# Kernel optimization log

Measured on AMD Instinct MI355X. Metric: run time of the kernel, lower is better.

Reference implementation:

```python
import jax, jax.numpy as jnp
import numpy as np

B, S, D = 2, 2048, 768
C = 8                # num_channels
R = D // C           # ternary_rank = 96 (RoPE head_dim)
THETA = 10000.0
TERNARY_STD = 0.2
TERNARY_SCALE = 1.0  # ternary_factor_scaling


def _rope_tables():
    # HF-style RoPE: inv_freq over half dim, emb = concat(freqs, freqs)
    inv_freq = 1.0 / (THETA ** (np.arange(0, R, 2, dtype=np.float32) / R))
    pos = np.arange(S, dtype=np.float32)
    freqs = pos[:, None] * inv_freq[None, :]          # [S, R/2]
    emb = np.concatenate([freqs, freqs], axis=-1)     # [S, R]
    cos = np.broadcast_to(np.cos(emb)[None], (B, S, R)).copy()
    sin = np.broadcast_to(np.sin(emb)[None], (B, S, R)).copy()
    return jnp.asarray(cos), jnp.asarray(sin)


def setup_inputs() -> dict:
    key = jax.random.key(0)
    k1, k2, k3 = jax.random.split(key, 3)
    qz = jax.random.normal(k1, (B, S, D), dtype=jnp.float32)
    U = jax.random.normal(k2, (D, D), dtype=jnp.float32) * TERNARY_STD
    V = jax.random.normal(k3, (D, D), dtype=jnp.float32) * TERNARY_STD
    cos, sin = _rope_tables()
    return {"qz": qz, "cos": cos, "sin": sin, "U": U, "V": V}


def _rotate_half(x):
    h = x.shape[-1] // 2
    return jnp.concatenate([-x[..., h:], x[..., :h]], axis=-1)


def reference(qz, cos, sin, U, V):
    # cos/sin: [B,S,R] -> broadcast over channel dim -> [B,1,S,R]
    cosb = cos[:, None, :, :]
    sinb = sin[:, None, :, :]
    rope = lambda x: x * cosb + _rotate_half(x) * sinb       # apply
    rope_o = lambda x: x * cosb - _rotate_half(x) * sinb     # apply_o (inverse)

    # projections: F.linear(qz, W) == qz @ W.T
    qz_u = (qz @ U.T * TERNARY_SCALE).reshape(B, S, C, R).transpose(0, 2, 1, 3)
    qz_v = (qz @ V.T * TERNARY_SCALE).reshape(B, S, C, R).transpose(0, 2, 1, 3)

    qz_uo = rope_o(qz_u)
    qz_ur = rope(qz_u)
    qz_vr = rope(qz_v)

    # message_F: [B,C,S,S]
    message_F = jnp.einsum('bcqr,bckr->bcqk', qz_ur, qz_vr)
    # softmax(message_F / regularize_h) with regularize_h = 1/D  ->  * D
    qh = jax.nn.softmax((message_F * jnp.float32(D)).astype(jnp.float32), axis=-1).astype(qz_ur.dtype)

    qh_v1 = rope_o(jnp.einsum('bcqk,bckr->bcqr', qh, qz_vr))  # qh @ qz_v
    qh_v2 = rope(jnp.einsum('bckq,bckr->bcqr', qh, qz_uo))    # qh^T @ qz_uo

    qh_v1 = qh_v1.transpose(0, 2, 1, 3).reshape(B, S, D)
    qh_v2 = qh_v2.transpose(0, 2, 1, 3).reshape(B, S, D)

    message_G = (qh_v1 @ U + qh_v2 @ V) * TERNARY_SCALE
    return message_G
```

## Files before the change

kernel.cpp:

```cpp
#include <hip/hip_runtime.h>

typedef _Float16 f16;
typedef _Float16 f16x8 __attribute__((ext_vector_type(8)));
typedef _Float16 f16x4 __attribute__((ext_vector_type(4)));
typedef float f32x4 __attribute__((ext_vector_type(4)));

#define MFMA16(A,B,C) __builtin_amdgcn_mfma_f32_16x16x32_f16(A,B,C,0,0,0)
#define INV2048 4.8828125e-4f
#define HN (16ll*2048*96)
#define UVN 589824
#define ZC1 1107.98979f
#define ZC2 0.54101064f

__device__ __forceinline__ void split_f16(float x, f16& h, f16& l) {
    h = (f16)x;
    l = (f16)((x - (float)h) * 2048.0f);
}

__global__ __launch_bounds__(256) void k0_split(const float* __restrict__ qz,
                                                const float* __restrict__ U,
                                                const float* __restrict__ V,
                                                f16* __restrict__ qzh, f16* __restrict__ qzl,
                                                f16* __restrict__ Uh, f16* __restrict__ Ul,
                                                f16* __restrict__ Vh, f16* __restrict__ Vl) {
    const int i4 = blockIdx.x * 256 + threadIdx.x;
    {
        float4 x = *(const float4*)(qz + (size_t)i4 * 4);
        f16 h0, l0, h1, l1, h2, l2, h3, l3;
        split_f16(x.x, h0, l0); split_f16(x.y, h1, l1);
        split_f16(x.z, h2, l2); split_f16(x.w, h3, l3);
        f16x4 hv = {h0, h1, h2, h3};
        f16x4 lv = {l0, l1, l2, l3};
        *(f16x4*)(qzh + (size_t)i4 * 4) = hv;
        *(f16x4*)(qzl + (size_t)i4 * 4) = lv;
    }
    if (i4 < UVN / 4) {
        float4 x = *(const float4*)(U + (size_t)i4 * 4);
        f16 h0, l0, h1, l1, h2, l2, h3, l3;
        split_f16(x.x, h0, l0); split_f16(x.y, h1, l1);
        split_f16(x.z, h2, l2); split_f16(x.w, h3, l3);
        f16x4 hv = {h0, h1, h2, h3};
        f16x4 lv = {l0, l1, l2, l3};
        *(f16x4*)(Uh + (size_t)i4 * 4) = hv;
        *(f16x4*)(Ul + (size_t)i4 * 4) = lv;
        float4 y = *(const float4*)(V + (size_t)i4 * 4);
        split_f16(y.x, h0, l0); split_f16(y.y, h1, l1);
        split_f16(y.z, h2, l2); split_f16(y.w, h3, l3);
        f16x4 hv2 = {h0, h1, h2, h3};
        f16x4 lv2 = {l0, l1, l2, l3};
        *(f16x4*)(Vh + (size_t)i4 * 4) = hv2;
        *(f16x4*)(Vl + (size_t)i4 * 4) = lv2;
    }
}

__global__ __launch_bounds__(256, 2) void k1_proj(const f16* __restrict__ qzh,
                                                  const f16* __restrict__ qzl,
                                                  const f16* __restrict__ Uh,
                                                  const f16* __restrict__ Ul,
                                                  const f16* __restrict__ Vh,
                                                  const f16* __restrict__ Vl,
                                                  const float* __restrict__ cosb,
                                                  const float* __restrict__ sinb,
                                                  f16* __restrict__ uhp, f16* __restrict__ ulp,
                                                  f16* __restrict__ vhp, f16* __restrict__ vlp,
                                                  f16* __restrict__ vT, f16* __restrict__ oT) {
    __shared__ __align__(16) f16 smem[36864];
    f16* sAh  = smem;
    f16* sAl  = smem + 4608;
    f16* sBuh = smem + 9216;
    f16* sBul = smem + 9216 + 6912;
    f16* sBvh = smem + 9216 + 2 * 6912;
    f16* sBvl = smem + 9216 + 3 * 6912;

    const int tid = threadIdx.x;
    const int w = tid >> 6, lane = tid & 63;
    const int quad = lane >> 4, l15 = lane & 15;
    const int wr = w >> 1, wc = w & 1;
    const int bs0 = blockIdx.x * 64;
    const int c = blockIdx.y;

    const f16* Ug_h = Uh + (size_t)c * 96 * 768;
    const f16* Ug_l = Ul + (size_t)c * 96 * 768;
    const f16* Vg_h = Vh + (size_t)c * 96 * 768;
    const f16* Vg_l = Vl + (size_t)c * 96 * 768;

    f32x4 aUS[2][3] = {}, aUX[2][3] = {};
    f32x4 aVS[2][3] = {}, aVX[2][3] = {};

    for (int k0 = 0; k0 < 768; k0 += 64) {
        __syncthreads();
#pragma unroll
        for (int m = 0; m < 2; ++m) {
            int f = tid + 256 * m, row = f >> 3, cg = f & 7;
            const size_t go = (size_t)(bs0 + row) * 768 + k0 + cg * 8;
            const int lo = row * 72 + cg * 8;
            *(float4*)&sAh[lo] = *(const float4*)(qzh + go);
            *(float4*)&sAl[lo] = *(const float4*)(qzl + go);
        }
#pragma unroll
        for (int m = 0; m < 3; ++m) {
            int f = tid + 256 * m, row = f >> 3, cg = f & 7;
            const size_t go = (size_t)row * 768 + k0 + cg * 8;
            const int lo = row * 72 + cg * 8;
            *(float4*)&sBuh[lo] = *(const float4*)(Ug_h + go);
            *(float4*)&sBul[lo] = *(const float4*)(Ug_l + go);
            *(float4*)&sBvh[lo] = *(const float4*)(Vg_h + go);
            *(float4*)&sBvl[lo] = *(const float4*)(Vg_l + go);
        }
        __syncthreads();
#pragma unroll
        for (int cc = 0; cc < 2; ++cc) {
            f16x8 ah[2], al[2];
#pragma unroll
            for (int mt = 0; mt < 2; ++mt) {
                const int ar = (32 * wr + 16 * mt + l15) * 72 + cc * 32 + quad * 8;
                ah[mt] = *(const f16x8*)&sAh[ar];
                al[mt] = *(const f16x8*)&sAl[ar];
            }
#pragma unroll
            for (int nt = 0; nt < 3; ++nt) {
                const int br = (48 * wc + 16 * nt + l15) * 72 + cc * 32 + quad * 8;
                f16x8 buh = *(const f16x8*)&sBuh[br];
                f16x8 bul = *(const f16x8*)&sBul[br];
                f16x8 bvh = *(const f16x8*)&sBvh[br];
                f16x8 bvl = *(const f16x8*)&sBvl[br];
#pragma unroll
                for (int mt = 0; mt < 2; ++mt) {
                    aUS[mt][nt] = MFMA16(ah[mt], buh, aUS[mt][nt]);
                    aUX[mt][nt] = MFMA16(ah[mt], bul, aUX[mt][nt]);
                    aUX[mt][nt] = MFMA16(al[mt], buh, aUX[mt][nt]);
                    aVS[mt][nt] = MFMA16(ah[mt], bvh, aVS[mt][nt]);
                    aVX[mt][nt] = MFMA16(ah[mt], bvl, aVX[mt][nt]);
                    aVX[mt][nt] = MFMA16(al[mt], bvh, aVX[mt][nt]);
                }
            }
        }
    }

    __syncthreads();
    float* LU = (float*)smem;
    float* LV = LU + 6400;
#pragma unroll
    for (int mt = 0; mt < 2; ++mt)
#pragma unroll
        for (int nt = 0; nt < 3; ++nt)
#pragma unroll
            for (int r = 0; r < 4; ++r) {
                const int sl = 32 * wr + 16 * mt + 4 * quad + r;
                const int col = 48 * wc + 16 * nt + l15;
                LU[sl * 100 + col] = aUS[mt][nt][r] + aUX[mt][nt][r] * INV2048;
                LV[sl * 100 + col] = aVS[mt][nt][r] + aVX[mt][nt][r] * INV2048;
            }
    __syncthreads();

    const int b = bs0 >> 11;
    const int s0 = bs0 & 2047;
    const int head = b * 8 + c;
    const size_t nb = (size_t)head * 2048 * 96;
    const size_t tb = (size_t)head * 96 * 2048;
    const int ty = tid >> 4, tx = tid & 15;

#pragma unroll
    for (int jj = 0; jj < 3; ++jj) {
        int r = tx + 16 * jj;
        f16 vt1[4], vt2[4], ot1[4], ot2[4];
#pragma unroll
        for (int ii = 0; ii < 4; ++ii) {
            int sl = 4 * ty + ii;
            int s = s0 + sl;
            int cbi = (b * 2048 + s) * 96 + r;
            float cc = cosb[cbi], ss = sinb[cbi];
            size_t rowb = nb + (size_t)s * 96;
            float u1 = LU[sl * 100 + r], u2 = LU[sl * 100 + r + 48];
            float v1 = LV[sl * 100 + r], v2 = LV[sl * 100 + r + 48];
            float ur1 = u1 * cc - u2 * ss, ur2 = u2 * cc + u1 * ss;
            float uo1 = u1 * cc + u2 * ss, uo2 = u2 * cc - u1 * ss;
            float vr1 = v1 * cc - v2 * ss, vr2 = v2 * cc + v1 * ss;
            f16 h, l;
            split_f16(ur1, h, l); uhp[rowb + r] = h;      ulp[rowb + r] = l;
            split_f16(ur2, h, l); uhp[rowb + r + 48] = h; ulp[rowb + r + 48] = l;
            split_f16(vr1, h, l); vhp[rowb + r] = h;      vlp[rowb + r] = l;      vt1[ii] = h;
            split_f16(vr2, h, l); vhp[rowb + r + 48] = h; vlp[rowb + r + 48] = l; vt2[ii] = h;
            ot1[ii] = (f16)uo1; ot2[ii] = (f16)uo2;
        }
        f16x4 pv1 = {vt1[0], vt1[1], vt1[2], vt1[3]};
        f16x4 pv2 = {vt2[0], vt2[1], vt2[2], vt2[3]};
        f16x4 po1 = {ot1[0], ot1[1], ot1[2], ot1[3]};
        f16x4 po2 = {ot2[0], ot2[1], ot2[2], ot2[3]};
        *(f16x4*)&vT[tb + (size_t)r * 2048 + s0 + 4 * ty] = pv1;
        *(f16x4*)&vT[tb + (size_t)(r + 48) * 2048 + s0 + 4 * ty] = pv2;
        *(f16x4*)&oT[tb + (size_t)r * 2048 + s0 + 4 * ty] = po1;
        *(f16x4*)&oT[tb + (size_t)(r + 48) * 2048 + s0 + 4 * ty] = po2;
    }
}

__global__ __launch_bounds__(256, 2) void k2_stats(const f16* __restrict__ uhp,
                                                   const f16* __restrict__ ulp,
                                                   const f16* __restrict__ vhp,
                                                   const f16* __restrict__ vlp,
                                                   float* __restrict__ Mo,
                                                   float* __restrict__ Lo) {
    __shared__ f16 Bh[64 * 104];
    __shared__ f16 Bl[64 * 104];
    __shared__ float Mbuf[4][64], Lbuf[4][64];
    const int tid = threadIdx.x, w = tid >> 6, lane = tid & 63;
    const int quad = lane >> 4, l15 = lane & 15;
    const int q0 = blockIdx.x * 64, head = blockIdx.y;
    const f16* Ah_g = uhp + (size_t)head * 2048 * 96;
    const f16* Al_g = ulp + (size_t)head * 2048 * 96;
    const f16* Bh_g = vhp + (size_t)head * 2048 * 96;
    const f16* Bl_g = vlp + (size_t)head * 2048 * 96;

    f16x8 Afh[4][3], Afl[4][3];
#pragma unroll
    for (int mt = 0; mt < 4; ++mt)
#pragma unroll
        for (int cc = 0; cc < 3; ++cc) {
            size_t off = (size_t)(q0 + 16 * mt + l15) * 96 + cc * 32 + quad * 8;
            Afh[mt][cc] = *(const f16x8*)(Ah_g + off);
            Afl[mt][cc] = *(const f16x8*)(Al_g + off);
        }

    float m_run[4][4], l_run[4][4];
#pragma unroll
    for (int mt = 0; mt < 4; ++mt)
#pragma unroll
        for (int r = 0; r < 4; ++r) { m_run[mt][r] = -3.0e38f; l_run[mt][r] = 0.f; }

    for (int k0 = 0; k0 < 2048; k0 += 64) {
        __syncthreads();
#pragma unroll
        for (int m = 0; m < 3; ++m) {
            int f = tid + 256 * m;
            int row = f / 12, c12 = f % 12;
            *(float4*)&Bh[row * 104 + c12 * 8] =
                *(const float4*)(Bh_g + (size_t)(k0 + row) * 96 + c12 * 8);
            *(float4*)&Bl[row * 104 + c12 * 8] =
                *(const float4*)(Bl_g + (size_t)(k0 + row) * 96 + c12 * 8);
        }
        __syncthreads();
        f32x4 accS[4] = {}, accX[4] = {};
#pragma unroll
        for (int cc = 0; cc < 3; ++cc) {
            f16x8 bh = *(const f16x8*)&Bh[(w * 16 + l15) * 104 + cc * 32 + quad * 8];
            f16x8 bl = *(const f16x8*)&Bl[(w * 16 + l15) * 104 + cc * 32 + quad * 8];
#pragma unroll
            for (int mt = 0; mt < 4; ++mt) {
                accS[mt] = MFMA16(Afh[mt][cc], bh, accS[mt]);
                accX[mt] = MFMA16(Afh[mt][cc], bl, accX[mt]);
                accX[mt] = MFMA16(Afl[mt][cc], bh, accX[mt]);
            }
        }
#pragma unroll
        for (int mt = 0; mt < 4; ++mt)
#pragma unroll
            for (int r = 0; r < 4; ++r) {
                float zl = fmaf(ZC1, accS[mt][r], ZC2 * accX[mt][r]);
                float nm = fmaxf(m_run[mt][r], zl);
                l_run[mt][r] = fmaf(l_run[mt][r], exp2f(m_run[mt][r] - nm),
                                    exp2f(zl - nm));
                m_run[mt][r] = nm;
            }
    }
#pragma unroll
    for (int mt = 0; mt < 4; ++mt)
#pragma unroll
        for (int r = 0; r < 4; ++r) {
            float m = m_run[mt][r], l = l_run[mt][r];
#pragma unroll
            for (int d = 1; d < 16; d <<= 1) {
                float mo = __shfl_xor(m, d), lo = __shfl_xor(l, d);
                float nm = fmaxf(m, mo);
                l = fmaf(l, exp2f(m - nm), lo * exp2f(mo - nm));
                m = nm;
            }
            m_run[mt][r] = m; l_run[mt][r] = l;
        }
    if (l15 == 0) {
#pragma unroll
        for (int mt = 0; mt < 4; ++mt)
#pragma unroll
            for (int r = 0; r < 4; ++r) {
                Mbuf[w][16 * mt + 4 * quad + r] = m_run[mt][r];
                Lbuf[w][16 * mt + 4 * quad + r] = l_run[mt][r];
            }
    }
    __syncthreads();
    if (tid < 64) {
        float M = -3.0e38f;
#pragma unroll
        for (int ww = 0; ww < 4; ++ww) M = fmaxf(M, Mbuf[ww][tid]);
        float L = 0.f;
#pragma unroll
        for (int ww = 0; ww < 4; ++ww) L += Lbuf[ww][tid] * exp2f(Mbuf[ww][tid] - M);
        Mo[head * 2048 + q0 + tid] = M;
        Lo[head * 2048 + q0 + tid] = L;
    }
}

__global__ __launch_bounds__(256, 2) void k3a(const f16* __restrict__ uhp,
                                              const f16* __restrict__ ulp,
                                              const f16* __restrict__ vhp,
                                              const f16* __restrict__ vlp,
                                              const f16* __restrict__ vT,
                                              const float* __restrict__ Mo,
                                              const float* __restrict__ Lo,
                                              const float* __restrict__ cosb,
                                              const float* __restrict__ sinb,
                                              f16* __restrict__ w1) {
    __shared__ f16 Bh[64 * 104];
    __shared__ f16 Bl[64 * 104];
    __shared__ f16 Vt[96 * 72];
    __shared__ f16 P[64 * 72];
    const int tid = threadIdx.x, w = tid >> 6, lane = tid & 63;
    const int quad = lane >> 4, l15 = lane & 15;
    const int q0 = blockIdx.x * 64, head = blockIdx.y;
    const f16* Ah_g = uhp + (size_t)head * 2048 * 96;
    const f16* Al_g = ulp + (size_t)head * 2048 * 96;
    const f16* Bh_g = vhp + (size_t)head * 2048 * 96;
    const f16* Bl_g = vlp + (size_t)head * 2048 * 96;
    const f16* Vt_g = vT + (size_t)head * 96 * 2048;

    f16x8 Afh[4][3], Afl[4][3];
#pragma unroll
    for (int mt = 0; mt < 4; ++mt)
#pragma unroll
        for (int cc = 0; cc < 3; ++cc) {
            size_t off = (size_t)(q0 + 16 * mt + l15) * 96 + cc * 32 + quad * 8;
            Afh[mt][cc] = *(const f16x8*)(Ah_g + off);
            Afl[mt][cc] = *(const f16x8*)(Al_g + off);
        }
    float negM[4][4];
#pragma unroll
    for (int mt = 0; mt < 4; ++mt)
#pragma unroll
        for (int r = 0; r < 4; ++r)
            negM[mt][r] = -Mo[head * 2048 + q0 + 16 * mt + 4 * quad + r];
    float invL[4];
#pragma unroll
    for (int r = 0; r < 4; ++r)
        invL[r] = 1.0f / Lo[head * 2048 + q0 + w * 16 + quad * 4 + r];

    f32x4 accO[6] = {};

    for (int k0 = 0; k0 < 2048; k0 += 64) {
        __syncthreads();
#pragma unroll
        for (int m = 0; m < 3; ++m) {
            int f = tid + 256 * m;
            int row = f / 12, c12 = f % 12;
            *(float4*)&Bh[row * 104 + c12 * 8] =
                *(const float4*)(Bh_g + (size_t)(k0 + row) * 96 + c12 * 8);
            *(float4*)&Bl[row * 104 + c12 * 8] =
                *(const float4*)(Bl_g + (size_t)(k0 + row) * 96 + c12 * 8);
        }
#pragma unroll
        for (int m = 0; m < 3; ++m) {
            int f = tid + 256 * m;
            int row = f >> 3, c8 = f & 7;
            *(float4*)&Vt[row * 72 + c8 * 8] =
                *(const float4*)(Vt_g + (size_t)row * 2048 + k0 + c8 * 8);
        }
        __syncthreads();
        f32x4 accS[4] = {}, accX[4] = {};
#pragma unroll
        for (int cc = 0; cc < 3; ++cc) {
            f16x8 bh = *(const f16x8*)&Bh[(w * 16 + l15) * 104 + cc * 32 + quad * 8];
            f16x8 bl = *(const f16x8*)&Bl[(w * 16 + l15) * 104 + cc * 32 + quad * 8];
#pragma unroll
            for (int mt = 0; mt < 4; ++mt) {
                accS[mt] = MFMA16(Afh[mt][cc], bh, accS[mt]);
                accX[mt] = MFMA16(Afh[mt][cc], bl, accX[mt]);
                accX[mt] = MFMA16(Afl[mt][cc], bh, accX[mt]);
            }
        }
#pragma unroll
        for (int mt = 0; mt < 4; ++mt)
#pragma unroll
            for (int r = 0; r < 4; ++r) {
                float zl = fmaf(ZC1, accS[mt][r], ZC2 * accX[mt][r]);
                P[(16 * mt + 4 * quad + r) * 72 + w * 16 + l15] =
                    (f16)exp2f(zl + negM[mt][r]);
            }
        __syncthreads();
#pragma unroll
        for (int kc = 0; kc < 2; ++kc) {
            f16x8 ap = *(const f16x8*)&P[(w * 16 + l15) * 72 + kc * 32 + quad * 8];
#pragma unroll
            for (int nt = 0; nt < 6; ++nt) {
                f16x8 bv = *(const f16x8*)&Vt[(nt * 16 + l15) * 72 + kc * 32 + quad * 8];
                accO[nt] = MFMA16(ap, bv, accO[nt]);
            }
        }
        __syncthreads();
    }
    const int b = head >> 3, c = head & 7;
#pragma unroll
    for (int r = 0; r < 4; ++r) {
        int q = q0 + w * 16 + quad * 4 + r;
        int cbi = (b * 2048 + q) * 96;
        f16* wrow = w1 + (size_t)(b * 2048 + q) * 768 + c * 96;
#pragma unroll
        for (int nt = 0; nt < 3; ++nt) {
            int rr = nt * 16 + l15;
            float cc = cosb[cbi + rr], ss = sinb[cbi + rr];
            float a = accO[nt][r] * invL[r];
            float b2 = accO[nt + 3][r] * invL[r];
            wrow[rr] = (f16)(a * cc + b2 * ss);
            wrow[rr + 48] = (f16)(b2 * cc - a * ss);
        }
    }
}

__global__ __launch_bounds__(256, 2) void k3b(const f16* __restrict__ uhp,
                                              const f16* __restrict__ ulp,
                                              const f16* __restrict__ vhp,
                                              const f16* __restrict__ vlp,
                                              const f16* __restrict__ oT,
                                              const float* __restrict__ Mo,
                                              const float* __restrict__ Lo,
                                              const float* __restrict__ cosb,
                                              const float* __restrict__ sinb,
                                              f16* __restrict__ w2) {
    __shared__ f16 Bh[64 * 104];
    __shared__ f16 Bl[64 * 104];
    __shared__ f16 Ot[96 * 72];
    __shared__ f16 P[64 * 72];
    const int tid = threadIdx.x, w = tid >> 6, lane = tid & 63;
    const int quad = lane >> 4, l15 = lane & 15;
    const int q0 = blockIdx.x * 64, head = blockIdx.y;
    const f16* Ah_g = vhp + (size_t)head * 2048 * 96;
    const f16* Al_g = vlp + (size_t)head * 2048 * 96;
    const f16* Bh_g = uhp + (size_t)head * 2048 * 96;
    const f16* Bl_g = ulp + (size_t)head * 2048 * 96;
    const f16* Ot_g = oT + (size_t)head * 96 * 2048;

    f16x8 Afh[4][3], Afl[4][3];
#pragma unroll
    for (int mt = 0; mt < 4; ++mt)
#pragma unroll
        for (int cc = 0; cc < 3; ++cc) {
            size_t off = (size_t)(q0 + 16 * mt + l15) * 96 + cc * 32 + quad * 8;
            Afh[mt][cc] = *(const f16x8*)(Ah_g + off);
            Afl[mt][cc] = *(const f16x8*)(Al_g + off);
        }

    f32x4 accO[6] = {};

    for (int k0 = 0; k0 < 2048; k0 += 64) {
        float negMk = -Mo[head * 2048 + k0 + w * 16 + l15];
        float invLk = 1.0f / Lo[head * 2048 + k0 + w * 16 + l15];
        __syncthreads();
#pragma unroll
        for (int m = 0; m < 3; ++m) {
            int f = tid + 256 * m;
            int row = f / 12, c12 = f % 12;
            *(float4*)&Bh[row * 104 + c12 * 8] =
                *(const float4*)(Bh_g + (size_t)(k0 + row) * 96 + c12 * 8);
            *(float4*)&Bl[row * 104 + c12 * 8] =
                *(const float4*)(Bl_g + (size_t)(k0 + row) * 96 + c12 * 8);
        }
#pragma unroll
        for (int m = 0; m < 3; ++m) {
            int f = tid + 256 * m;
            int row = f >> 3, c8 = f & 7;
            *(float4*)&Ot[row * 72 + c8 * 8] =
                *(const float4*)(Ot_g + (size_t)row * 2048 + k0 + c8 * 8);
        }
        __syncthreads();
        f32x4 accS[4] = {}, accX[4] = {};
#pragma unroll
        for (int cc = 0; cc < 3; ++cc) {
            f16x8 bh = *(const f16x8*)&Bh[(w * 16 + l15) * 104 + cc * 32 + quad * 8];
            f16x8 bl = *(const f16x8*)&Bl[(w * 16 + l15) * 104 + cc * 32 + quad * 8];
#pragma unroll
            for (int mt = 0; mt < 4; ++mt) {
                accS[mt] = MFMA16(Afh[mt][cc], bh, accS[mt]);
                accX[mt] = MFMA16(Afl[mt][cc], bh, accX[mt]);
                accX[mt] = MFMA16(Afh[mt][cc], bl, accX[mt]);
            }
        }
#pragma unroll
        for (int mt = 0; mt < 4; ++mt)
#pragma unroll
            for (int r = 0; r < 4; ++r) {
                float zl = fmaf(ZC1, accS[mt][r], ZC2 * accX[mt][r]);
                P[(16 * mt + 4 * quad + r) * 72 + w * 16 + l15] =
                    (f16)(exp2f(zl + negMk) * invLk);
            }
        __syncthreads();
#pragma unroll
        for (int kc = 0; kc < 2; ++kc) {
            f16x8 ap = *(const f16x8*)&P[(w * 16 + l15) * 72 + kc * 32 + quad * 8];
#pragma unroll
            for (int nt = 0; nt < 6; ++nt) {
                f16x8 bo = *(const f16x8*)&Ot[(nt * 16 + l15) * 72 + kc * 32 + quad * 8];
                accO[nt] = MFMA16(ap, bo, accO[nt]);
            }
        }
        __syncthreads();
    }
    const int b = head >> 3, c = head & 7;
#pragma unroll
    for (int r = 0; r < 4; ++r) {
        int q = q0 + w * 16 + quad * 4 + r;
        int cbi = (b * 2048 + q) * 96;
        f16* wrow = w2 + (size_t)(b * 2048 + q) * 768 + c * 96;
#pragma unroll
        for (int nt = 0; nt < 3; ++nt) {
            int rr = nt * 16 + l15;
            float cc = cosb[cbi + rr], ss = sinb[cbi + rr];
            float a = accO[nt][r];
            float b2 = accO[nt + 3][r];
            wrow[rr] = (f16)(a * cc - b2 * ss);
            wrow[rr + 48] = (f16)(b2 * cc + a * ss);
        }
    }
}

__global__ __launch_bounds__(256, 2) void k4_final(const f16* __restrict__ w1,
                                                   const f16* __restrict__ w2,
                                                   const float* __restrict__ U,
                                                   const float* __restrict__ V,
                                                   float* __restrict__ outp) {
    __shared__ f16 A1[128 * 56];
    __shared__ f16 A2[128 * 56];
    __shared__ f16 B1[64 * 56];
    __shared__ f16 B2[64 * 56];
    const int tid = threadIdx.x, w = tid >> 6, lane = tid & 63;
    const int quad = lane >> 4, l15 = lane & 15;
    const int bs0 = blockIdx.x * 128;
    const int d0 = blockIdx.y * 64;
    f32x4 acc[2][4] = {};

    for (int ec = 0; ec < 24; ++ec) {
        int e0 = ec * 32;
        __syncthreads();
#pragma unroll
        for (int m = 0; m < 2; ++m) {
            int f = tid + 256 * m;
            int row = f >> 2, q = f & 3;
            *(float4*)&A1[row * 56 + q * 8] =
                *(const float4*)(w1 + (size_t)(bs0 + row) * 768 + e0 + q * 8);
            *(float4*)&A2[row * 56 + q * 8] =
                *(const float4*)(w2 + (size_t)(bs0 + row) * 768 + e0 + q * 8);
        }
#pragma unroll
        for (int m2 = 0; m2 < 2; ++m2) {
            int e_r = (tid >> 4) + 16 * m2;
            int dc = tid & 15;
            float4 fu = *(const float4*)(U + (size_t)(e0 + e_r) * 768 + d0 + dc * 4);
            float4 fv = *(const float4*)(V + (size_t)(e0 + e_r) * 768 + d0 + dc * 4);
            B1[(dc * 4 + 0) * 56 + e_r] = (f16)fu.x;
            B1[(dc * 4 + 1) * 56 + e_r] = (f16)fu.y;
            B1[(dc * 4 + 2) * 56 + e_r] = (f16)fu.z;
            B1[(dc * 4 + 3) * 56 + e_r] = (f16)fu.w;
            B2[(dc * 4 + 0) * 56 + e_r] = (f16)fv.x;
            B2[(dc * 4 + 1) * 56 + e_r] = (f16)fv.y;
            B2[(dc * 4 + 2) * 56 + e_r] = (f16)fv.z;
            B2[(dc * 4 + 3) * 56 + e_r] = (f16)fv.w;
        }
        __syncthreads();
        f16x8 a1f[2], a2f[2];
#pragma unroll
        for (int mt = 0; mt < 2; ++mt) {
            a1f[mt] = *(const f16x8*)&A1[(32 * w + 16 * mt + l15) * 56 + quad * 8];
            a2f[mt] = *(const f16x8*)&A2[(32 * w + 16 * mt + l15) * 56 + quad * 8];
        }
#pragma unroll
        for (int nt = 0; nt < 4; ++nt) {
            f16x8 b1f = *(const f16x8*)&B1[(nt * 16 + l15) * 56 + quad * 8];
            f16x8 b2f = *(const f16x8*)&B2[(nt * 16 + l15) * 56 + quad * 8];
#pragma unroll
            for (int mt = 0; mt < 2; ++mt) {
                acc[mt][nt] = MFMA16(a1f[mt], b1f, acc[mt][nt]);
                acc[mt][nt] = MFMA16(a2f[mt], b2f, acc[mt][nt]);
            }
        }
    }
#pragma unroll
    for (int mt = 0; mt < 2; ++mt)
#pragma unroll
        for (int nt = 0; nt < 4; ++nt)
#pragma unroll
            for (int r = 0; r < 4; ++r) {
                int s = bs0 + 32 * w + 16 * mt + 4 * quad + r;
                int d = d0 + 16 * nt + l15;
                outp[(size_t)s * 768 + d] = acc[mt][nt][r];
            }
}

extern "C" void kernel_launch(void* const* d_in, const int* in_sizes, int n_in,
                              void* d_out, int out_size, void* d_ws, size_t ws_size,
                              hipStream_t stream) {
    const float* qz   = (const float*)d_in[0];
    const float* cosb = (const float*)d_in[1];
    const float* sinb = (const float*)d_in[2];
    const float* U    = (const float*)d_in[3];
    const float* V    = (const float*)d_in[4];
    float* outp = (float*)d_out;

    f16* ws16 = (f16*)d_ws;
    f16* uhp = ws16;
    f16* ulp = ws16 + HN;
    f16* vhp = ws16 + 2 * HN;
    f16* vlp = ws16 + 3 * HN;
    f16* vT  = ws16 + 4 * HN;
    f16* oT  = ws16 + 5 * HN;
    f16* w1  = ws16 + 6 * HN;
    f16* w2  = ws16 + 7 * HN;
    float* Mo = (float*)(ws16 + 8 * HN);
    float* Lo = Mo + 16 * 2048;

    f16* qzh = w1;
    f16* qzl = w2;
    f16* outw = (f16*)d_out;
    f16* Uh = outw;
    f16* Ul = outw + UVN;
    f16* Vh = outw + 2 * UVN;
    f16* Vl = outw + 3 * UVN;

    k0_split<<<dim3(3072), 256, 0, stream>>>(qz, U, V, qzh, qzl, Uh, Ul, Vh, Vl);
    k1_proj<<<dim3(64, 8), 256, 0, stream>>>(qzh, qzl, Uh, Ul, Vh, Vl, cosb, sinb,
                                             uhp, ulp, vhp, vlp, vT, oT);
    k2_stats<<<dim3(32, 16), 256, 0, stream>>>(uhp, ulp, vhp, vlp, Mo, Lo);
    k3a<<<dim3(32, 16), 256, 0, stream>>>(uhp, ulp, vhp, vlp, vT, Mo, Lo, cosb, sinb, w1);
    k3b<<<dim3(32, 16), 256, 0, stream>>>(uhp, ulp, vhp, vlp, oT, Mo, Lo, cosb, sinb, w2);
    k4_final<<<dim3(32, 12), 256, 0, stream>>>(w1, w2, U, V, outp);
}
```

Measured before the change: 364.8 us.

## Compute softmax row sums in PV MFMA via ones column, max-only stats pass

The stats kernel now computes only the row maximum, dropping the online-softmax rescaling and its two exp2 calls per score element. The row sum is instead obtained in k3a by appending a 16-row tile of ones to the V^T shared tile, so one extra MFMA output tile accumulates sum(P). k3a then normalizes from that accumulator and writes Lo, which k3b reads afterwards on the same stream. The cost is one more MFMA tile per step and slightly more shared memory in k3a, and the sum now comes from the f16-rounded P values.

```diff
diff --git a/kernel.cpp b/kernel.cpp
--- a/kernel.cpp
+++ b/kernel.cpp
@@ -198,11 +198,10 @@
                                                    const f16* __restrict__ ulp,
                                                    const f16* __restrict__ vhp,
                                                    const f16* __restrict__ vlp,
-                                                   float* __restrict__ Mo,
-                                                   float* __restrict__ Lo) {
+                                                   float* __restrict__ Mo) {
     __shared__ f16 Bh[64 * 104];
     __shared__ f16 Bl[64 * 104];
-    __shared__ float Mbuf[4][64], Lbuf[4][64];
+    __shared__ float Mbuf[4][64];
     const int tid = threadIdx.x, w = tid >> 6, lane = tid & 63;
     const int quad = lane >> 4, l15 = lane & 15;
     const int q0 = blockIdx.x * 64, head = blockIdx.y;
@@ -221,11 +220,11 @@
             Afl[mt][cc] = *(const f16x8*)(Al_g + off);
         }
 
-    float m_run[4][4], l_run[4][4];
+    float m_run[4][4];
 #pragma unroll
     for (int mt = 0; mt < 4; ++mt)
 #pragma unroll
-        for (int r = 0; r < 4; ++r) { m_run[mt][r] = -3.0e38f; l_run[mt][r] = 0.f; }
+        for (int r = 0; r < 4; ++r) m_run[mt][r] = -3.0e38f;
 
     for (int k0 = 0; k0 < 2048; k0 += 64) {
         __syncthreads();
@@ -256,45 +255,31 @@
 #pragma unroll
             for (int r = 0; r < 4; ++r) {
                 float zl = fmaf(ZC1, accS[mt][r], ZC2 * accX[mt][r]);
-                float nm = fmaxf(m_run[mt][r], zl);
-                l_run[mt][r] = fmaf(l_run[mt][r], exp2f(m_run[mt][r] - nm),
-                                    exp2f(zl - nm));
-                m_run[mt][r] = nm;
+                m_run[mt][r] = fmaxf(m_run[mt][r], zl);
             }
     }
 #pragma unroll
     for (int mt = 0; mt < 4; ++mt)
 #pragma unroll
         for (int r = 0; r < 4; ++r) {
-            float m = m_run[mt][r], l = l_run[mt][r];
-#pragma unroll
-            for (int d = 1; d < 16; d <<= 1) {
-                float mo = __shfl_xor(m, d), lo = __shfl_xor(l, d);
-                float nm = fmaxf(m, mo);
-                l = fmaf(l, exp2f(m - nm), lo * exp2f(mo - nm));
-                m = nm;
-            }
-            m_run[mt][r] = m; l_run[mt][r] = l;
+            float m = m_run[mt][r];
+            m = fmaxf(m, __shfl_xor(m, 1)); m = fmaxf(m, __shfl_xor(m, 2));
+            m = fmaxf(m, __shfl_xor(m, 4)); m = fmaxf(m, __shfl_xor(m, 8));
+            m_run[mt][r] = m;
         }
     if (l15 == 0) {
 #pragma unroll
         for (int mt = 0; mt < 4; ++mt)
 #pragma unroll
-            for (int r = 0; r < 4; ++r) {
+            for (int r = 0; r < 4; ++r)
                 Mbuf[w][16 * mt + 4 * quad + r] = m_run[mt][r];
-                Lbuf[w][16 * mt + 4 * quad + r] = l_run[mt][r];
-            }
     }
     __syncthreads();
     if (tid < 64) {
         float M = -3.0e38f;
 #pragma unroll
         for (int ww = 0; ww < 4; ++ww) M = fmaxf(M, Mbuf[ww][tid]);
-        float L = 0.f;
-#pragma unroll
-        for (int ww = 0; ww < 4; ++ww) L += Lbuf[ww][tid] * exp2f(Mbuf[ww][tid] - M);
         Mo[head * 2048 + q0 + tid] = M;
-        Lo[head * 2048 + q0 + tid] = L;
     }
 }
 
@@ -304,13 +289,13 @@
                                               const f16* __restrict__ vlp,
                                               const f16* __restrict__ vT,
                                               const float* __restrict__ Mo,
-                                              const float* __restrict__ Lo,
+                                              float* __restrict__ Lo,
                                               const float* __restrict__ cosb,
                                               const float* __restrict__ sinb,
                                               f16* __restrict__ w1) {
     __shared__ f16 Bh[64 * 104];
     __shared__ f16 Bl[64 * 104];
-    __shared__ f16 Vt[96 * 72];
+    __shared__ f16 Vt[112 * 72];
     __shared__ f16 P[64 * 72];
     const int tid = threadIdx.x, w = tid >> 6, lane = tid & 63;
     const int quad = lane >> 4, l15 = lane & 15;
@@ -336,12 +321,14 @@
 #pragma unroll
         for (int r = 0; r < 4; ++r)
             negM[mt][r] = -Mo[head * 2048 + q0 + 16 * mt + 4 * quad + r];
-    float invL[4];
-#pragma unroll
-    for (int r = 0; r < 4; ++r)
-        invL[r] = 1.0f / Lo[head * 2048 + q0 + w * 16 + quad * 4 + r];
-
-    f32x4 accO[6] = {};
+
+    if (tid < 144) {
+        f16x8 ones = {(f16)1, (f16)1, (f16)1, (f16)1,
+                      (f16)1, (f16)1, (f16)1, (f16)1};
+        *(f16x8*)&Vt[96 * 72 + tid * 8] = ones;
+    }
+
+    f32x4 accO[7] = {};
 
     for (int k0 = 0; k0 < 2048; k0 += 64) {
         __syncthreads();
@@ -387,13 +374,22 @@
         for (int kc = 0; kc < 2; ++kc) {
             f16x8 ap = *(const f16x8*)&P[(w * 16 + l15) * 72 + kc * 32 + quad * 8];
 #pragma unroll
-            for (int nt = 0; nt < 6; ++nt) {
+            for (int nt = 0; nt < 7; ++nt) {
                 f16x8 bv = *(const f16x8*)&Vt[(nt * 16 + l15) * 72 + kc * 32 + quad * 8];
                 accO[nt] = MFMA16(ap, bv, accO[nt]);
             }
         }
         __syncthreads();
     }
+    float invL[4];
+#pragma unroll
+    for (int r = 0; r < 4; ++r) invL[r] = 1.0f / accO[6][r];
+    if (l15 == 0) {
+#pragma unroll
+        for (int r = 0; r < 4; ++r)
+            Lo[head * 2048 + q0 + w * 16 + quad * 4 + r] = accO[6][r];
+    }
+
     const int b = head >> 3, c = head & 7;
 #pragma unroll
     for (int r = 0; r < 4; ++r) {
@@ -623,7 +619,7 @@
     k0_split<<<dim3(3072), 256, 0, stream>>>(qz, U, V, qzh, qzl, Uh, Ul, Vh, Vl);
     k1_proj<<<dim3(64, 8), 256, 0, stream>>>(qzh, qzl, Uh, Ul, Vh, Vl, cosb, sinb,
                                              uhp, ulp, vhp, vlp, vT, oT);
-    k2_stats<<<dim3(32, 16), 256, 0, stream>>>(uhp, ulp, vhp, vlp, Mo, Lo);
+    k2_stats<<<dim3(32, 16), 256, 0, stream>>>(uhp, ulp, vhp, vlp, Mo);
     k3a<<<dim3(32, 16), 256, 0, stream>>>(uhp, ulp, vhp, vlp, vT, Mo, Lo, cosb, sinb, w1);
     k3b<<<dim3(32, 16), 256, 0, stream>>>(uhp, ulp, vhp, vlp, oT, Mo, Lo, cosb, sinb, w2);
     k4_final<<<dim3(32, 12), 256, 0, stream>>>(w1, w2, U, V, outp);
```

New measurement: 339.8 us. 1.07x faster.
